# Performance work log

Hardware: AMD Instinct MI355X
Metric: run time of the kernel (lower is better)

## Reference

```python
import jax, jax.numpy as jnp
import numpy as np

V, E, H, A, B, S = 32000, 1024, 1024, 1024, 64, 512

def setup_inputs() -> dict:
    key = jax.random.key(0)
    ks = jax.random.split(key, 20)
    sc = lambda d: 1.0 / np.sqrt(d)
    return {
        "x": jax.random.randint(ks[0], (B,), 0, V),
        "encoder_outputs": jax.random.normal(ks[1], (S, B, H), jnp.float32),
        "h0": jax.random.normal(ks[2], (1, B, H), jnp.float32),
        "c0": jax.random.normal(ks[3], (1, B, H), jnp.float32),
        "Wa": jax.random.normal(ks[4], (A, H), jnp.float32) * sc(H),
        "b_wa": jnp.zeros((A,), jnp.float32),
        "Ua": jax.random.normal(ks[5], (A, H), jnp.float32) * sc(H),
        "b_ua": jnp.zeros((A,), jnp.float32),
        "va": jax.random.normal(ks[6], (1, A), jnp.float32) * sc(A),
        "b_va": jnp.zeros((1,), jnp.float32),
        "emb": jax.random.normal(ks[7], (V, E), jnp.float32) * 0.02,
        "W_ih": jax.random.normal(ks[8], (4 * H, E + H), jnp.float32) * sc(E + H),
        "W_hh": jax.random.normal(ks[9], (4 * H, H), jnp.float32) * sc(H),
        "b_ih": jnp.zeros((4 * H,), jnp.float32),
        "b_hh": jnp.zeros((4 * H,), jnp.float32),
        "W_clf": jax.random.normal(ks[10], (V, H), jnp.float32) * sc(H),
        "b_clf": jnp.zeros((V,), jnp.float32),
    }

def reference(x, encoder_outputs, h0, c0, Wa, b_wa, Ua, b_ua, va, b_va, emb,
              W_ih, W_hh, b_ih, b_hh, W_clf, b_clf):
    # Bahdanau additive attention: scores over time (axis 0)
    tmp1 = jnp.einsum('lbh,ah->lba', h0, Wa) + b_wa            # [1,B,A]
    tmp2 = jnp.einsum('sbh,ah->sba', encoder_outputs, Ua) + b_ua  # [S,B,A]
    scores = jnp.einsum('sba,oa->sbo', jnp.tanh(tmp1 + tmp2), va) + b_va  # [S,B,1]
    w = jax.nn.softmax(scores, axis=0)                          # softmax over S
    ctx = jnp.einsum('sb,sbh->bh', w[..., 0], encoder_outputs)  # [B,H]
    # embed token, concat with context
    inp = jnp.concatenate([emb[x], ctx], axis=-1)               # [B,E+H]
    # single LSTM step (PyTorch gate order i,f,g,o)
    gates = inp @ W_ih.T + b_ih + h0[0] @ W_hh.T + b_hh         # [B,4H]
    i, f, g, o = jnp.split(gates, 4, axis=-1)
    c1 = jax.nn.sigmoid(f) * c0[0] + jax.nn.sigmoid(i) * jnp.tanh(g)
    h1 = jax.nn.sigmoid(o) * jnp.tanh(c1)
    logits = h1 @ W_clf.T + b_clf                               # [B,V]
    return jax.nn.log_softmax(logits, axis=-1)[None]            # [1,B,V]
```

## Files before the change

### kernel.cpp

```cpp
#include <hip/hip_runtime.h>
#include <hip/hip_bf16.h>
#include <math.h>

typedef unsigned short u16;
typedef unsigned int u32;
typedef __attribute__((ext_vector_type(4))) float f32x4;
typedef __attribute__((ext_vector_type(8))) short s16x8;
typedef __attribute__((ext_vector_type(8))) unsigned short u16x8;

#define DEV __device__ __forceinline__


DEV u16 f2bf(float f) {
    union { float f; u32 u; } x{f};
    return (u16)((x.u + 0x7FFFu + ((x.u >> 16) & 1u)) >> 16);
}
DEV float bf2f(u16 h) {
    union { u32 u; float f; } x;
    x.u = ((u32)h) << 16;
    return x.f;
}
DEV float sigm(float x) { return 1.0f / (1.0f + __expf(-x)); }
DEV float tanh_f(float x) {
    float c = fminf(fmaxf(x, -9.0f), 9.0f);
    float e = __expf(2.0f * c);
    return (e - 1.0f) / (e + 1.0f);
}

#define GLL16(g, l) __builtin_amdgcn_global_load_lds( \
    (const __attribute__((address_space(1))) u32*)(g), \
    (__attribute__((address_space(3))) u32*)(l), 16, 0, 0)

__global__ void kzero(float* p, int n) {
    int i = blockIdx.x * blockDim.x + threadIdx.x;
    if (i < n) p[i] = 0.0f;
}

__global__ void kcvt8(const float* __restrict__ in, u16* __restrict__ out, int n8) {
    int i = blockIdx.x * blockDim.x + threadIdx.x;
    if (i >= n8) return;
    float4 f0 = ((const float4*)in)[i * 2];
    float4 f1 = ((const float4*)in)[i * 2 + 1];
    u16x8 o = {f2bf(f0.x), f2bf(f0.y), f2bf(f0.z), f2bf(f0.w),
               f2bf(f1.x), f2bf(f1.y), f2bf(f1.z), f2bf(f1.w)};
    ((u16x8*)out)[i] = o;
}

__global__ __launch_bounds__(256, 2) void kscores128(
    const u16* __restrict__ encbf, const u16* __restrict__ Uabf,
    const float* __restrict__ tmp1c, const float* __restrict__ va,
    float* __restrict__ scores)
{
    __shared__ __align__(16) u16 shm[16896];

    int wg  = blockIdx.x;
    int lin = (wg & 7) * 256 + (wg >> 3);
    int mt  = lin >> 3, nt = lin & 7;

    int t = threadIdx.x;
    int wid = t >> 6, lane = t & 63;
    int wr = wid >> 1, wc = wid & 1;
    int lr = lane & 15, lg = lane >> 4;

    f32x4 acc[4][4];
#pragma unroll
    for (int i = 0; i < 4; i++)
#pragma unroll
        for (int j = 0; j < 4; j++) acc[i][j] = (f32x4){0.f, 0.f, 0.f, 0.f};

    int srow = t >> 3;
    int sq   = ((t & 7) ^ (srow & 7)) * 8;
    const u16* asrc = encbf + (size_t)(mt * 128 + srow) * 1024 + sq;
    const u16* bsrc = Uabf + (size_t)(nt * 128 + srow) * 1024 + sq;
    u16* As = shm;
    u16* Bs = shm + 8192;

    const u16* A0 = &shm[(wr * 64 + lr) * 64];
    const u16* B0 = &shm[8192 + (wc * 64 + lr) * 64];
    int o0 = (lg * 8) ^ ((lr & 7) * 8);
    int o1 = (32 + lg * 8) ^ ((lr & 7) * 8);

    for (int k0 = 0; k0 < 1024; k0 += 64) {
        __syncthreads();
#pragma unroll
        for (int r = 0; r < 4; r++) {
            GLL16(asrc + k0 + (size_t)r * 32 * 1024, As + r * 2048 + t * 8);
            GLL16(bsrc + k0 + (size_t)r * 32 * 1024, Bs + r * 2048 + t * 8);
        }
        __syncthreads();

        s16x8 af[4], bf[4];
#pragma unroll
        for (int i = 0; i < 4; i++) af[i] = *(const s16x8*)(A0 + i * 1024 + o0);
#pragma unroll
        for (int j = 0; j < 4; j++) bf[j] = *(const s16x8*)(B0 + j * 1024 + o0);
#pragma unroll
        for (int i = 0; i < 4; i++)
#pragma unroll
            for (int j = 0; j < 4; j++)
                acc[i][j] = __builtin_amdgcn_mfma_f32_16x16x32_bf16(af[i], bf[j], acc[i][j], 0, 0, 0);
#pragma unroll
        for (int i = 0; i < 4; i++) af[i] = *(const s16x8*)(A0 + i * 1024 + o1);
#pragma unroll
        for (int j = 0; j < 4; j++) bf[j] = *(const s16x8*)(B0 + j * 1024 + o1);
#pragma unroll
        for (int i = 0; i < 4; i++)
#pragma unroll
            for (int j = 0; j < 4; j++)
                acc[i][j] = __builtin_amdgcn_mfma_f32_16x16x32_bf16(af[i], bf[j], acc[i][j], 0, 0, 0);
    }

    __syncthreads();
    float* ltmp = (float*)shm;
    for (int i2 = t; i2 < 8192; i2 += 256) {
        int b = i2 >> 7, a = i2 & 127;
        ltmp[b * 132 + a] = tmp1c[b * 1024 + nt * 128 + a];
    }
    __syncthreads();

    float vaj[4];
#pragma unroll
    for (int j = 0; j < 4; j++) vaj[j] = va[nt * 128 + wc * 64 + j * 16 + lr];

#pragma unroll
    for (int i = 0; i < 4; i++) {
        float rs[4] = {0.f, 0.f, 0.f, 0.f};
        int rowloc = wr * 64 + i * 16 + lg * 4;
#pragma unroll
        for (int j = 0; j < 4; j++) {
            int al = wc * 64 + j * 16 + lr;
#pragma unroll
            for (int r = 0; r < 4; r++) {
                int b = (rowloc + r) & 63;
                rs[r] += vaj[j] * tanh_f(acc[i][j][r] + ltmp[b * 132 + al]);
            }
        }
#pragma unroll
        for (int m = 1; m < 16; m <<= 1)
#pragma unroll
            for (int r = 0; r < 4; r++) rs[r] += __shfl_xor(rs[r], m, 64);
        if (lr == 0) {
            int mrow = mt * 128 + rowloc;
#pragma unroll
            for (int r = 0; r < 4; r++) atomicAdd(&scores[mrow + r], rs[r]);
        }
    }
}

__global__ __launch_bounds__(256) void kskinny(
    const u16* __restrict__ Abf, int Ktot,
    const float* __restrict__ B1, int K1,
    const float* __restrict__ B2,
    float* __restrict__ Cout, int N, int klen)
{
    __shared__ u16 As[64 * 40];
    __shared__ u16 Bs[128 * 40];

    int nt = blockIdx.x, p = blockIdx.y;
    int t = threadIdx.x;
    int wid = t >> 6, lane = t & 63;
    int lr = lane & 15, lg = lane >> 4;
    int K2 = Ktot - K1;

    f32x4 acc[4][2];
#pragma unroll
    for (int i = 0; i < 4; i++)
#pragma unroll
        for (int j = 0; j < 2; j++) acc[i][j] = (f32x4){0.f, 0.f, 0.f, 0.f};

    int arow = t >> 2, aq = t & 3;
    const u16* ap = Abf + (size_t)arow * Ktot + aq * 8;
    u16* asw = &As[arow * 40 + aq * 8];

    int brow = t >> 1, bhalf = t & 1;
    int n = nt * 128 + brow;
    u16* bsw = &Bs[brow * 40 + bhalf * 16];

    int kbeg = p * klen, kend = kbeg + klen;
    for (int k0 = kbeg; k0 < kend; k0 += 32) {
        __syncthreads();
        *(uint4*)asw = *(const uint4*)(ap + k0);
        int kk = k0 + bhalf * 16;
        const float* bp = (kk < K1) ? (B1 + (size_t)n * K1 + kk)
                                    : (B2 + (size_t)n * K2 + (kk - K1));
        float4 b0 = ((const float4*)bp)[0];
        float4 b1 = ((const float4*)bp)[1];
        float4 b2 = ((const float4*)bp)[2];
        float4 b3 = ((const float4*)bp)[3];
        u16x8 q0 = {f2bf(b0.x), f2bf(b0.y), f2bf(b0.z), f2bf(b0.w),
                    f2bf(b1.x), f2bf(b1.y), f2bf(b1.z), f2bf(b1.w)};
        u16x8 q1 = {f2bf(b2.x), f2bf(b2.y), f2bf(b2.z), f2bf(b2.w),
                    f2bf(b3.x), f2bf(b3.y), f2bf(b3.z), f2bf(b3.w)};
        *(u16x8*)bsw = q0;
        *(u16x8*)(bsw + 8) = q1;
        __syncthreads();

        const u16* abase = &As[lr * 40 + lg * 8];
        const u16* bbase = &Bs[(wid * 32 + lr) * 40 + lg * 8];
        s16x8 af[4], bfr[2];
#pragma unroll
        for (int i = 0; i < 4; i++) af[i]  = *(const s16x8*)(abase + i * 16 * 40);
#pragma unroll
        for (int j = 0; j < 2; j++) bfr[j] = *(const s16x8*)(bbase + j * 16 * 40);
#pragma unroll
        for (int i = 0; i < 4; i++)
#pragma unroll
            for (int j = 0; j < 2; j++)
                acc[i][j] = __builtin_amdgcn_mfma_f32_16x16x32_bf16(af[i], bfr[j], acc[i][j], 0, 0, 0);
    }

#pragma unroll
    for (int i = 0; i < 4; i++)
#pragma unroll
        for (int j = 0; j < 2; j++) {
            int m = i * 16 + lg * 4;
            int col = nt * 128 + wid * 32 + j * 16 + lr;
#pragma unroll
            for (int r = 0; r < 4; r++)
                Cout[((size_t)(p * 64 + m + r)) * N + col] = acc[i][j][r];
        }
}

__global__ void kredbias(const float* __restrict__ part, const float* __restrict__ bias1,
                         const float* __restrict__ bias2, float* __restrict__ out,
                         int N, int P)
{
    int idx = blockIdx.x * blockDim.x + threadIdx.x;
    if (idx >= 64 * N) return;
    int n = idx % N;
    float v = bias1[n] + bias2[n];
    for (int p = 0; p < P; p++) v += part[(size_t)p * 64 * N + idx];
    out[idx] = v;
}

__global__ __launch_bounds__(512) void ksoftmax_w(const float* __restrict__ scores,
                                                  float* __restrict__ w)
{
    int b = blockIdx.x, s = threadIdx.x;
    __shared__ float red[8], red2[8];
    float v = scores[s * 64 + b];
    float m = v;
#pragma unroll
    for (int mask = 1; mask < 64; mask <<= 1) m = fmaxf(m, __shfl_xor(m, mask, 64));
    if ((s & 63) == 0) red[s >> 6] = m;
    __syncthreads();
#pragma unroll
    for (int k = 0; k < 8; k++) m = fmaxf(m, red[k]);
    float e = __expf(v - m);
    float sum = e;
#pragma unroll
    for (int mask = 1; mask < 64; mask <<= 1) sum += __shfl_xor(sum, mask, 64);
    if ((s & 63) == 0) red2[s >> 6] = sum;
    __syncthreads();
    sum = 0.f;
#pragma unroll
    for (int k = 0; k < 8; k++) sum += red2[k];
    w[s * 64 + b] = e / sum;
}

__global__ __launch_bounds__(256) void kctx(const u16* __restrict__ encbf,
                                            const float* __restrict__ w,
                                            float* __restrict__ pctx)
{
    int b = blockIdx.x & 63, ch = blockIdx.x >> 6;
    int h4 = threadIdx.x;
    float4 acc = {0.f, 0.f, 0.f, 0.f};
    int s0 = ch * 64;
#pragma unroll 4
    for (int si = 0; si < 64; si++) {
        int s = s0 + si;
        float wv = w[s * 64 + b];
        ushort4 e = ((const ushort4*)(encbf + ((size_t)(s * 64 + b)) * 1024))[h4];
        acc.x += wv * bf2f(e.x); acc.y += wv * bf2f(e.y);
        acc.z += wv * bf2f(e.z); acc.w += wv * bf2f(e.w);
    }
    ((float4*)pctx)[((size_t)(ch * 64 + b)) * 256 + h4] = acc;
}

__global__ void kbuild(const int* __restrict__ x, const float* __restrict__ emb,
                       const float* __restrict__ pctx, const float* __restrict__ h0,
                       u16* __restrict__ inp2bf)
{
    int idx = blockIdx.x * blockDim.x + threadIdx.x;
    if (idx >= 64 * 3072) return;
    int b = idx / 3072, k = idx % 3072;
    float v;
    if (k < 1024) {
        v = emb[(size_t)x[b] * 1024 + k];
    } else if (k < 2048) {
        int h = k - 1024;
        v = 0.f;
        for (int p = 0; p < 8; p++) v += pctx[(size_t)(p * 64 + b) * 1024 + h];
    } else {
        v = h0[b * 1024 + (k - 2048)];
    }
    inp2bf[idx] = f2bf(v);
}

__global__ void klstm(const float* __restrict__ gp, const float* __restrict__ b_ih,
                      const float* __restrict__ b_hh, const float* __restrict__ c0,
                      u16* __restrict__ h1bf)
{
    int idx = blockIdx.x * blockDim.x + threadIdx.x;
    int b = idx >> 10, j = idx & 1023;
    float ig = b_ih[j] + b_hh[j];
    float fg = b_ih[1024 + j] + b_hh[1024 + j];
    float gg = b_ih[2048 + j] + b_hh[2048 + j];
    float og = b_ih[3072 + j] + b_hh[3072 + j];
    for (int p = 0; p < 8; p++) {
        const float* g = gp + ((size_t)p * 64 + b) * 4096;
        ig += g[j]; fg += g[1024 + j]; gg += g[2048 + j]; og += g[3072 + j];
    }
    float c = sigm(fg) * c0[idx] + sigm(ig) * tanh_f(gg);
    float h = sigm(og) * tanh_f(c);
    h1bf[idx] = f2bf(h);
}

__global__ __launch_bounds__(1024) void klogsoftmax(const float* __restrict__ lp,
                                                    const float* __restrict__ b_clf,
                                                    float* __restrict__ out)
{
    int b = blockIdx.x, t = threadIdx.x;
    __shared__ float red[16], red2[16];
    float v[32];
    float mx = -1e30f;
#pragma unroll
    for (int i = 0; i < 32; i++) {
        int idx = t + i * 1024;
        if (idx < 32000) {
            float s = b_clf[idx];
#pragma unroll
            for (int p = 0; p < 4; p++)
                s += lp[((size_t)(p * 64 + b)) * 32000 + idx];
            v[i] = s;
            mx = fmaxf(mx, v[i]);
        } else v[i] = -1e30f;
    }
#pragma unroll
    for (int mask = 1; mask < 64; mask <<= 1) mx = fmaxf(mx, __shfl_xor(mx, mask, 64));
    if ((t & 63) == 0) red[t >> 6] = mx;
    __syncthreads();
#pragma unroll
    for (int k = 0; k < 16; k++) mx = fmaxf(mx, red[k]);
    float s = 0.f;
#pragma unroll
    for (int i = 0; i < 32; i++) {
        int idx = t + i * 1024;
        if (idx < 32000) s += __expf(v[i] - mx);
    }
#pragma unroll
    for (int mask = 1; mask < 64; mask <<= 1) s += __shfl_xor(s, mask, 64);
    if ((t & 63) == 0) red2[t >> 6] = s;
    __syncthreads();
    s = 0.f;
#pragma unroll
    for (int k = 0; k < 16; k++) s += red2[k];
    float lse = mx + logf(s);
#pragma unroll
    for (int i = 0; i < 32; i++) {
        int idx = t + i * 1024;
        if (idx < 32000) out[(size_t)b * 32000 + idx] = v[i] - lse;
    }
}

extern "C" void kernel_launch(void* const* d_in, const int* in_sizes, int n_in,
                              void* d_out, int out_size, void* d_ws, size_t ws_size,
                              hipStream_t stream)
{
    const int*   x     = (const int*)d_in[0];
    const float* enc   = (const float*)d_in[1];
    const float* h0    = (const float*)d_in[2];
    const float* c0    = (const float*)d_in[3];
    const float* Wa    = (const float*)d_in[4];
    const float* b_wa  = (const float*)d_in[5];
    const float* Ua    = (const float*)d_in[6];
    const float* b_ua  = (const float*)d_in[7];
    const float* va    = (const float*)d_in[8];
    const float* emb   = (const float*)d_in[10];
    const float* W_ih  = (const float*)d_in[11];
    const float* W_hh  = (const float*)d_in[12];
    const float* b_ih  = (const float*)d_in[13];
    const float* b_hh  = (const float*)d_in[14];
    const float* W_clf = (const float*)d_in[15];
    const float* b_clf = (const float*)d_in[16];
    float* out = (float*)d_out;

    char* ws = (char*)d_ws;
    u16*   encbf    = (u16*)  (ws + 0);
    float* gparts   = (float*)(ws + 0);
    float* lparts   = (float*)(ws + 8388608);
    float* scores   = (float*)(ws + 67108864);
    float* wbuf     = (float*)(ws + 67239936);
    float* tmp1part = (float*)(ws + 67371008);
    float* tmp1c    = (float*)(ws + 69468160);
    u16*   h0bf     = (u16*)  (ws + 69730304);
    u16*   Uabf     = (u16*)  (ws + 69861376);
    float* pctx     = (float*)(ws + 71958528);
    u16*   inp2bf   = (u16*)  (ws + 74055680);
    u16*   h1bf     = (u16*)  (ws + 74448896);

    kzero<<<128, 256, 0, stream>>>(scores, 32768);
    kcvt8<<<16384, 256, 0, stream>>>(enc, encbf, 33554432 / 8);
    kcvt8<<<512, 256, 0, stream>>>(Ua, Uabf, 1048576 / 8);
    kcvt8<<<32, 256, 0, stream>>>(h0, h0bf, 65536 / 8);

    {
        dim3 g(8, 8);
        kskinny<<<g, 256, 0, stream>>>(h0bf, 1024, Wa, 1024, nullptr, tmp1part, 1024, 128);
    }
    kredbias<<<256, 256, 0, stream>>>(tmp1part, b_wa, b_ua, tmp1c, 1024, 8);

    kscores128<<<2048, 256, 0, stream>>>(encbf, Uabf, tmp1c, va, scores);
    ksoftmax_w<<<64, 512, 0, stream>>>(scores, wbuf);
    kctx<<<512, 256, 0, stream>>>(encbf, wbuf, pctx);
    kbuild<<<768, 256, 0, stream>>>(x, emb, pctx, h0, inp2bf);

    {
        dim3 g(32, 8);
        kskinny<<<g, 256, 0, stream>>>(inp2bf, 3072, W_ih, 2048, W_hh, gparts, 4096, 384);
    }
    klstm<<<256, 256, 0, stream>>>(gparts, b_ih, b_hh, c0, h1bf);

    {
        dim3 g(250, 4);
        kskinny<<<g, 256, 0, stream>>>(h1bf, 1024, W_clf, 1024, nullptr, lparts, 32000, 256);
    }
    klogsoftmax<<<64, 1024, 0, stream>>>(lparts, b_clf, out);
}
```

Before: 240.8 us.

## Rewrite attention-score GEMM as 256x256 tile with double-buffered async loads

Replaces the 128x128-tile scores kernel (256 threads, 2048 blocks) with a 256x256-tile kernel using 512 threads and 512 blocks. The new kernel double-buffers LDS (128 KB) and interleaves global-to-LDS loads for upcoming K tiles with MFMA phases, using explicit waitcnt, barriers and setprio. The aim is higher arithmetic intensity and hiding load latency behind compute in the dominant GEMM. In exchange, occupancy drops to one block per CU, and the hand-tuned synchronisation is fragile.

```diff
diff --git a/kernel.cpp b/kernel.cpp
--- a/kernel.cpp
+++ b/kernel.cpp
@@ -46,93 +46,144 @@
     ((u16x8*)out)[i] = o;
 }
 
-__global__ __launch_bounds__(256, 2) void kscores128(
+
+template<int F0>
+DEV void mmq(f32x4 (&acc)[8][4], const s16x8 (&af)[2][2], const s16x8 (&bfrag)[4][2]) {
+#pragma unroll
+    for (int f = 0; f < 2; f++)
+#pragma unroll
+        for (int j = 0; j < 4; j++) {
+            acc[F0 + f][j] = __builtin_amdgcn_mfma_f32_16x16x32_bf16(af[f][0], bfrag[j][0], acc[F0 + f][j], 0, 0, 0);
+            acc[F0 + f][j] = __builtin_amdgcn_mfma_f32_16x16x32_bf16(af[f][1], bfrag[j][1], acc[F0 + f][j], 0, 0, 0);
+        }
+}
+
+__global__ __launch_bounds__(512, 1) void kscores256v2(
     const u16* __restrict__ encbf, const u16* __restrict__ Uabf,
     const float* __restrict__ tmp1c, const float* __restrict__ va,
     float* __restrict__ scores)
 {
-    __shared__ __align__(16) u16 shm[16896];
+    __shared__ __align__(16) u16 shm[65536];
 
     int wg  = blockIdx.x;
-    int lin = (wg & 7) * 256 + (wg >> 3);
-    int mt  = lin >> 3, nt = lin & 7;
+    int lin = (wg & 7) * 64 + (wg >> 3);
+    int mt  = lin >> 2, nt = lin & 3;
 
     int t = threadIdx.x;
     int wid = t >> 6, lane = t & 63;
-    int wr = wid >> 1, wc = wid & 1;
+    int wm = wid >> 2, wn = wid & 3;
     int lr = lane & 15, lg = lane >> 4;
 
-    f32x4 acc[4][4];
-#pragma unroll
-    for (int i = 0; i < 4; i++)
+    f32x4 acc[8][4];
+#pragma unroll
+    for (int i = 0; i < 8; i++)
 #pragma unroll
         for (int j = 0; j < 4; j++) acc[i][j] = (f32x4){0.f, 0.f, 0.f, 0.f};
 
     int srow = t >> 3;
-    int sq   = ((t & 7) ^ (srow & 7)) * 8;
-    const u16* asrc = encbf + (size_t)(mt * 128 + srow) * 1024 + sq;
-    const u16* bsrc = Uabf + (size_t)(nt * 128 + srow) * 1024 + sq;
-    u16* As = shm;
-    u16* Bs = shm + 8192;
-
-    const u16* A0 = &shm[(wr * 64 + lr) * 64];
-    const u16* B0 = &shm[8192 + (wc * 64 + lr) * 64];
-    int o0 = (lg * 8) ^ ((lr & 7) * 8);
-    int o1 = (32 + lg * 8) ^ ((lr & 7) * 8);
-
-    for (int k0 = 0; k0 < 1024; k0 += 64) {
-        __syncthreads();
-#pragma unroll
-        for (int r = 0; r < 4; r++) {
-            GLL16(asrc + k0 + (size_t)r * 32 * 1024, As + r * 2048 + t * 8);
-            GLL16(bsrc + k0 + (size_t)r * 32 * 1024, Bs + r * 2048 + t * 8);
-        }
-        __syncthreads();
-
-        s16x8 af[4], bf[4];
-#pragma unroll
-        for (int i = 0; i < 4; i++) af[i] = *(const s16x8*)(A0 + i * 1024 + o0);
-#pragma unroll
-        for (int j = 0; j < 4; j++) bf[j] = *(const s16x8*)(B0 + j * 1024 + o0);
-#pragma unroll
-        for (int i = 0; i < 4; i++)
-#pragma unroll
-            for (int j = 0; j < 4; j++)
-                acc[i][j] = __builtin_amdgcn_mfma_f32_16x16x32_bf16(af[i], bf[j], acc[i][j], 0, 0, 0);
-#pragma unroll
-        for (int i = 0; i < 4; i++) af[i] = *(const s16x8*)(A0 + i * 1024 + o1);
-#pragma unroll
-        for (int j = 0; j < 4; j++) bf[j] = *(const s16x8*)(B0 + j * 1024 + o1);
-#pragma unroll
-        for (int i = 0; i < 4; i++)
-#pragma unroll
-            for (int j = 0; j < 4; j++)
-                acc[i][j] = __builtin_amdgcn_mfma_f32_16x16x32_bf16(af[i], bf[j], acc[i][j], 0, 0, 0);
-    }
-
+    int sq8  = ((t & 7) ^ (srow & 7)) * 8;
+    const u16* asrcb = encbf + (size_t)(mt * 256 + srow) * 1024 + sq8;
+    const u16* bsrcb = Uabf + (size_t)(nt * 256 + srow) * 1024 + sq8;
+
+#define STG_A(SE, RB, KO) GLL16(asrcb + (size_t)(RB) * 1024 + (KO), shm + (SE) + (RB) * 64 + t * 8)
+#define STG_B(SE, RB, KO) GLL16(bsrcb + (size_t)(RB) * 1024 + (KO), shm + (SE) + 16384 + (RB) * 64 + t * 8)
+
+    const u16* Abase = shm + (wm * 128 + lr) * 64;
+    const u16* Bbase = shm + 16384 + (wn * 64 + lr) * 64;
+    int xor8 = (lr & 7) * 8;
+    int o0 = (lg * 8) ^ xor8;
+    int o1 = (32 + lg * 8) ^ xor8;
+
+    s16x8 af[2][2], bfrag[4][2];
+
+#define RD_A2(F0, AB) { \
+    af[0][0] = *(const s16x8*)((AB) + (F0) * 1024 + o0); \
+    af[0][1] = *(const s16x8*)((AB) + (F0) * 1024 + o1); \
+    af[1][0] = *(const s16x8*)((AB) + (F0 + 1) * 1024 + o0); \
+    af[1][1] = *(const s16x8*)((AB) + (F0 + 1) * 1024 + o1); }
+
+#define PHTAIL(F0) \
+    __builtin_amdgcn_s_barrier(); \
+    asm volatile("s_waitcnt lgkmcnt(0)" ::: "memory"); \
+    __builtin_amdgcn_sched_barrier(0); \
+    __builtin_amdgcn_s_setprio(1); \
+    mmq<F0>(acc, af, bfrag); \
+    __builtin_amdgcn_s_setprio(0); \
+    __builtin_amdgcn_s_barrier(); \
+    __builtin_amdgcn_sched_barrier(0);
+
+    STG_B(0, 0, 0);  STG_B(0, 64, 0);  STG_B(0, 128, 0); STG_B(0, 192, 0);
+    STG_A(0, 0, 0);  STG_A(0, 128, 0); STG_A(0, 64, 0);  STG_A(0, 192, 0);
+    STG_B(32768, 0, 64);  STG_B(32768, 64, 64);
+    STG_B(32768, 128, 64); STG_B(32768, 192, 64);
+    STG_A(32768, 0, 64);  STG_A(32768, 128, 64);
+    asm volatile("s_waitcnt vmcnt(6)" ::: "memory");
+    __builtin_amdgcn_s_barrier();
+    __builtin_amdgcn_sched_barrier(0);
+
+#define TILE_BODY(T, SB, SBX) { \
+    int kA = ((T) + 2 < 16 ? (T) + 2 : 15) * 64; \
+    int kH = ((T) + 1 < 16 ? (T) + 1 : 15) * 64; \
+    const u16* Ab = Abase + (SB); \
+    const u16* Bb = Bbase + (SB); \
+     \
+    _Pragma("unroll") \
+    for (int j = 0; j < 4; j++) { \
+        bfrag[j][0] = *(const s16x8*)(Bb + j * 1024 + o0); \
+        bfrag[j][1] = *(const s16x8*)(Bb + j * 1024 + o1); \
+    } \
+    RD_A2(0, Ab); \
+    STG_A((SBX), 64, kH); STG_A((SBX), 192, kH); \
+    PHTAIL(0); \
+     \
+    RD_A2(2, Ab); \
+    STG_B((SB), 0, kA); STG_B((SB), 64, kA); \
+    PHTAIL(2); \
+     \
+    RD_A2(4, Ab); \
+    STG_B((SB), 128, kA); STG_B((SB), 192, kA); \
+    PHTAIL(4); \
+     \
+    RD_A2(6, Ab); \
+    STG_A((SB), 0, kA); STG_A((SB), 128, kA); \
+    asm volatile("s_waitcnt vmcnt(6)" ::: "memory"); \
+    PHTAIL(6); \
+}
+
+    for (int tt = 0; tt < 8; tt++) {
+        int T0 = tt * 2;
+        TILE_BODY(T0, 0, 32768);
+        TILE_BODY(T0 + 1, 32768, 0);
+    }
+
+    asm volatile("s_waitcnt vmcnt(0)" ::: "memory");
+    __builtin_amdgcn_s_barrier();
+    __builtin_amdgcn_sched_barrier(0);
+
+    float* ltmp = (float*)shm;
+#pragma unroll
+    for (int i = 0; i < 8; i++) {
+        int idx = t + i * 512;
+        int row = idx >> 6, c4 = idx & 63;
+        float4 v = *(const float4*)(tmp1c + row * 1024 + nt * 256 + c4 * 4);
+        *(float4*)(ltmp + row * 260 + c4 * 4) = v;
+    }
     __syncthreads();
-    float* ltmp = (float*)shm;
-    for (int i2 = t; i2 < 8192; i2 += 256) {
-        int b = i2 >> 7, a = i2 & 127;
-        ltmp[b * 132 + a] = tmp1c[b * 1024 + nt * 128 + a];
-    }
-    __syncthreads();
 
     float vaj[4];
 #pragma unroll
-    for (int j = 0; j < 4; j++) vaj[j] = va[nt * 128 + wc * 64 + j * 16 + lr];
-
-#pragma unroll
-    for (int i = 0; i < 4; i++) {
+    for (int j = 0; j < 4; j++) vaj[j] = va[nt * 256 + wn * 64 + j * 16 + lr];
+
+#pragma unroll
+    for (int fi = 0; fi < 8; fi++) {
         float rs[4] = {0.f, 0.f, 0.f, 0.f};
-        int rowloc = wr * 64 + i * 16 + lg * 4;
 #pragma unroll
         for (int j = 0; j < 4; j++) {
-            int al = wc * 64 + j * 16 + lr;
+            int ac = wn * 64 + j * 16 + lr;
 #pragma unroll
             for (int r = 0; r < 4; r++) {
-                int b = (rowloc + r) & 63;
-                rs[r] += vaj[j] * tanh_f(acc[i][j][r] + ltmp[b * 132 + al]);
+                int b = (fi * 16 + lg * 4 + r) & 63;
+                rs[r] += vaj[j] * tanh_f(acc[fi][j][r] + ltmp[b * 260 + ac]);
             }
         }
 #pragma unroll
@@ -140,11 +191,16 @@
 #pragma unroll
             for (int r = 0; r < 4; r++) rs[r] += __shfl_xor(rs[r], m, 64);
         if (lr == 0) {
-            int mrow = mt * 128 + rowloc;
+            int mrow = mt * 256 + wm * 128 + fi * 16 + lg * 4;
 #pragma unroll
             for (int r = 0; r < 4; r++) atomicAdd(&scores[mrow + r], rs[r]);
         }
     }
+#undef STG_A
+#undef STG_B
+#undef RD_A2
+#undef PHTAIL
+#undef TILE_BODY
 }
 
 __global__ __launch_bounds__(256) void kskinny(
@@ -410,7 +466,7 @@
     }
     kredbias<<<256, 256, 0, stream>>>(tmp1part, b_wa, b_ua, tmp1c, 1024, 8);
 
-    kscores128<<<2048, 256, 0, stream>>>(encbf, Uabf, tmp1c, va, scores);
+    kscores256v2<<<512, 512, 0, stream>>>(encbf, Uabf, tmp1c, va, scores);
     ksoftmax_w<<<64, 512, 0, stream>>>(scores, wbuf);
     kctx<<<512, 256, 0, stream>>>(encbf, wbuf, pctx);
     kbuild<<<768, 256, 0, stream>>>(x, emb, pctx, h0, inp2bf);
```

Result: faster. 233.2 us (-3.2%).
